# Performance work log

Hardware: AMD Instinct MI355X
Metric: run time of the kernel (lower is better)

Reference implementation:

```python
import jax, jax.numpy as jnp
import numpy as np

B, L, H_IN, H_RED, H_MLP = 2, 1024, 768, 128, 256

def setup_inputs() -> dict:
    key = jax.random.key(0)
    ks = jax.random.split(key, 7)
    s_in = 1.0 / np.sqrt(H_IN)
    s_p = 1.0 / np.sqrt(2 * H_RED)
    s_m = 1.0 / np.sqrt(H_MLP)
    return {
        "inputs": jax.random.normal(ks[0], (B, L, H_IN), dtype=jnp.float32),
        "Wr": jax.random.uniform(ks[1], (H_RED, H_IN), jnp.float32, -s_in, s_in),
        "br": jax.random.uniform(ks[2], (H_RED,), jnp.float32, -s_in, s_in),
        "W1": jax.random.uniform(ks[3], (H_MLP, 2 * H_RED), jnp.float32, -s_p, s_p),
        "b1": jax.random.uniform(ks[4], (H_MLP,), jnp.float32, -s_p, s_p),
        "W2": jax.random.uniform(ks[5], (1, H_MLP), jnp.float32, -s_m, s_m),
        "b2": jax.random.uniform(ks[6], (1,), jnp.float32, -s_m, s_m),
    }

def reference(inputs, Wr, br, W1, b1, W2, b2):
    # pre_reduction: [B,L,H_IN] -> [B,L,H_RED]
    e = jnp.einsum("blh,rh->blr", inputs, Wr) + br
    b_, l_, r_ = e.shape
    # pairwise concat: row i gets e[i], col j gets e[j] -> [B,L,L,2R]
    row = jnp.broadcast_to(e[:, :, None, :], (b_, l_, l_, r_))
    col = jnp.broadcast_to(e[:, None, :, :], (b_, l_, l_, r_))
    pair = jnp.concatenate([row, col], axis=-1)
    # Lin2D: Linear(2R,256) -> ReLU -> Linear(256,1)
    h = jax.nn.relu(jnp.einsum("bijc,mc->bijm", pair, W1) + b1)
    out = jnp.einsum("bijm,om->bijo", h, W2) + b2  # [B,L,L,1]
    out = out[..., 0]  # [B,L,L]
    # symmetrize: triu(out) + triu(out,1)^T
    upper = jnp.triu(out)
    lower = jnp.swapaxes(jnp.triu(out, k=1), -1, -2)
    return upper + lower
```

## Files before the change

### kernel.cpp

```cpp
#include <hip/hip_runtime.h>

typedef __attribute__((ext_vector_type(4))) float f32x4;
typedef __attribute__((ext_vector_type(8))) short bf16x8;

__device__ inline unsigned short f2bf(float x) {
  unsigned u = __builtin_bit_cast(unsigned, x);
  u += 0x7fffu + ((u >> 16) & 1u);
  return (unsigned short)(u >> 16);
}

__device__ inline bf16x8 pack8(f32x4 lo, f32x4 hi) {
  bf16x8 r;
  r[0] = (short)f2bf(lo[0]); r[1] = (short)f2bf(lo[1]);
  r[2] = (short)f2bf(lo[2]); r[3] = (short)f2bf(lo[3]);
  r[4] = (short)f2bf(hi[0]); r[5] = (short)f2bf(hi[1]);
  r[6] = (short)f2bf(hi[2]); r[7] = (short)f2bf(hi[3]);
  return r;
}

__global__ __launch_bounds__(256) void prep_kernel(
    const float* __restrict__ X, const float* __restrict__ Wr,
    const float* __restrict__ W1, const float* __restrict__ W2,
    unsigned short* __restrict__ Xbf, unsigned short* __restrict__ Wrbf,
    unsigned short* __restrict__ W1bf, float* __restrict__ w2h) {
  int bid = blockIdx.x, tid = threadIdx.x;
  if (bid < 768) {
    size_t o = (size_t)bid * 2048 + tid * 8;
    f32x4 a = *(const f32x4*)(X + o), b = *(const f32x4*)(X + o + 4);
    *(bf16x8*)(Xbf + o) = pack8(a, b);
  } else if (bid < 816) {
    size_t o = (size_t)(bid - 768) * 2048 + tid * 8;
    f32x4 a = *(const f32x4*)(Wr + o), b = *(const f32x4*)(Wr + o + 4);
    *(bf16x8*)(Wrbf + o) = pack8(a, b);
  } else if (bid < 848) {
    size_t o = (size_t)(bid - 816) * 2048 + tid * 8;
    int m = (int)(o >> 7), k = (int)(o & 127);
    const float* src = (m < 256) ? (W1 + (size_t)m * 256 + k)
                                 : (W1 + (size_t)(m - 256) * 256 + 128 + k);
    f32x4 a = *(const f32x4*)src, b = *(const f32x4*)(src + 4);
    *(bf16x8*)(W1bf + o) = pack8(a, b);
  } else {
    w2h[tid] = 0.5f * W2[tid];
  }
}

__global__ __launch_bounds__(256) void gemm1_kernel(
    const unsigned short* __restrict__ Xbf, const unsigned short* __restrict__ Wrbf,
    const float* __restrict__ br, unsigned short* __restrict__ Ebf) {
  int wave = threadIdx.x >> 6, lane = threadIdx.x & 63;
  int tok0 = (blockIdx.x * 4 + wave) * 16;
  int n0 = blockIdx.y * 64;
  int lr = lane & 15, kg = (lane >> 4) * 8;
  const unsigned short* ap = Xbf + (size_t)(tok0 + lr) * 768 + kg;
  const unsigned short* bp0 = Wrbf + (size_t)(n0 + lr) * 768 + kg;
  const unsigned short* bp1 = bp0 + 16 * 768;
  const unsigned short* bp2 = bp0 + 32 * 768;
  const unsigned short* bp3 = bp0 + 48 * 768;
  f32x4 acc0 = {0,0,0,0}, acc1 = {0,0,0,0}, acc2 = {0,0,0,0}, acc3 = {0,0,0,0};
#pragma unroll 4
  for (int k0 = 0; k0 < 768; k0 += 32) {
    bf16x8 a = *(const bf16x8*)(ap + k0);
    bf16x8 b0 = *(const bf16x8*)(bp0 + k0);
    bf16x8 b1 = *(const bf16x8*)(bp1 + k0);
    bf16x8 b2 = *(const bf16x8*)(bp2 + k0);
    bf16x8 b3 = *(const bf16x8*)(bp3 + k0);
    acc0 = __builtin_amdgcn_mfma_f32_16x16x32_bf16(a, b0, acc0, 0, 0, 0);
    acc1 = __builtin_amdgcn_mfma_f32_16x16x32_bf16(a, b1, acc1, 0, 0, 0);
    acc2 = __builtin_amdgcn_mfma_f32_16x16x32_bf16(a, b2, acc2, 0, 0, 0);
    acc3 = __builtin_amdgcn_mfma_f32_16x16x32_bf16(a, b3, acc3, 0, 0, 0);
  }
  int rb = (lane >> 4) * 4;
  f32x4 accs[4] = {acc0, acc1, acc2, acc3};
#pragma unroll
  for (int t = 0; t < 4; ++t) {
    int n = n0 + t * 16 + lr;
    float bias = br[n];
#pragma unroll
    for (int r = 0; r < 4; ++r)
      Ebf[(size_t)(tok0 + rb + r) * 128 + n] = f2bf(accs[t][r] + bias);
  }
}

__global__ __launch_bounds__(256) void gemm2_kernel(
    const unsigned short* __restrict__ Ebf, const unsigned short* __restrict__ W1bf,
    const float* __restrict__ b1, const float* __restrict__ w2h,
    float* __restrict__ UVt, float* __restrict__ cvec) {
  int wave = threadIdx.x >> 6, lane = threadIdx.x & 63;
  int t0 = blockIdx.x * 64;
  int m0 = (blockIdx.y * 4 + wave) * 16;
  int lr = lane & 15, kg = (lane >> 4) * 8;
  const unsigned short* aB = W1bf + (size_t)(m0 + lr) * 128 + kg;
  f32x4 acc[4] = {{0,0,0,0},{0,0,0,0},{0,0,0,0},{0,0,0,0}};
#pragma unroll
  for (int k0 = 0; k0 < 128; k0 += 32) {
    bf16x8 a = *(const bf16x8*)(aB + k0);
#pragma unroll
    for (int t = 0; t < 4; ++t) {
      bf16x8 b = *(const bf16x8*)(Ebf + (size_t)(t0 + t * 16 + lr) * 128 + kg + k0);
      acc[t] = __builtin_amdgcn_mfma_f32_16x16x32_bf16(a, b, acc[t], 0, 0, 0);
    }
  }
  int rb = (lane >> 4) * 4;
  float p[4] = {0.f, 0.f, 0.f, 0.f};
#pragma unroll
  for (int t = 0; t < 4; ++t) {
#pragma unroll
    for (int r = 0; r < 4; ++r) {
      int m = m0 + rb + r;
      float val = acc[t][r] + ((m0 < 256) ? b1[m] : 0.f);
      UVt[(size_t)m * 2048 + t0 + t * 16 + lr] = val;
      p[t] = fmaf(w2h[m & 255], val, p[t]);
    }
  }
#pragma unroll
  for (int t = 0; t < 4; ++t) {
    p[t] += __shfl_xor(p[t], 16);
    p[t] += __shfl_xor(p[t], 32);
  }
  if (lane < 16) {
    int h = (m0 < 256) ? 0 : 1;
#pragma unroll
    for (int t = 0; t < 4; ++t)
      atomicAdd(&cvec[h * 2048 + t0 + t * 16 + lane], p[t]);
  }
}

__global__ __launch_bounds__(256) void pairwise_kernel(
    const float* __restrict__ UVt, const float* __restrict__ w2h,
    const float* __restrict__ cvec, const float* __restrict__ b2p,
    float* __restrict__ Out) {
  __shared__ float u_s[4][64][36];
  __shared__ float v_s[4][64][36];
  __shared__ float w2_s[256];
  __shared__ float cuv[64];

  int tid = threadIdx.x;
  int wave = tid >> 6, lane = tid & 63;
  int b = blockIdx.y;
  int p = blockIdx.x;
  int it = 0;
  while (p >= 32 - it) { p -= 32 - it; ++it; }
  int jt = it + p;

  int utok = b * 1024 + it * 32;
  int vtok = b * 1024 + jt * 32;

  w2_s[tid] = w2h[tid];
  if (tid < 32) cuv[tid] = cvec[utok + tid];
  else if (tid < 64) cuv[tid] = cvec[2048 + vtok + (tid - 32)];

  int mr = lane >> 3, tq = (lane & 7) * 4;
#pragma unroll
  for (int g = 0; g < 8; ++g) {
    int ml = g * 8 + mr;
    int m = wave * 64 + ml;
    *(f32x4*)&u_s[wave][ml][tq] = *(const f32x4*)(UVt + (size_t)m * 2048 + utok + tq);
    *(f32x4*)&v_s[wave][ml][tq] = *(const f32x4*)(UVt + (size_t)(256 + m) * 2048 + vtok + tq);
  }
  __syncthreads();

  int tx = lane & 7, ty = lane >> 3;
  float acc[4][4] = {{0,0,0,0},{0,0,0,0},{0,0,0,0},{0,0,0,0}};
  for (int ml = 0; ml < 64; ml += 4) {
    f32x4 wq = *(const f32x4*)&w2_s[wave * 64 + ml];
#pragma unroll
    for (int s = 0; s < 4; ++s) {
      f32x4 uu = *(const f32x4*)&u_s[wave][ml + s][4 * ty];
      f32x4 vv = *(const f32x4*)&v_s[wave][ml + s][4 * tx];
      float w = wq[s];
#pragma unroll
      for (int i = 0; i < 4; ++i)
#pragma unroll
        for (int j = 0; j < 4; ++j)
          acc[i][j] = fmaf(w, fabsf(uu[i] + vv[j]), acc[i][j]);
    }
  }

  __syncthreads();
  float* ov = (float*)u_s;
  if (wave > 0) {
#pragma unroll
    for (int i = 0; i < 4; ++i) {
      f32x4 rowv = {acc[i][0], acc[i][1], acc[i][2], acc[i][3]};
      *(f32x4*)&ov[(((wave - 1) * 4 + i) * 64 + lane) * 4] = rowv;
    }
  }
  __syncthreads();
  if (wave == 0) {
#pragma unroll
    for (int w = 1; w < 4; ++w)
#pragma unroll
      for (int i = 0; i < 4; ++i) {
        f32x4 rowv = *(const f32x4*)&ov[(((w - 1) * 4 + i) * 64 + lane) * 4];
#pragma unroll
        for (int j = 0; j < 4; ++j) acc[i][j] += rowv[j];
      }
    float b2v = b2p[0];
    float val[4][4];
#pragma unroll
    for (int i = 0; i < 4; ++i)
#pragma unroll
      for (int j = 0; j < 4; ++j)
        val[i][j] = acc[i][j] + cuv[4 * ty + i] + cuv[32 + 4 * tx + j] + b2v;

    size_t obase = (size_t)b << 20;
    int i0 = it * 32, j0 = jt * 32;
    if (it != jt) {
#pragma unroll
      for (int i = 0; i < 4; ++i) {
        f32x4 dv = {val[i][0], val[i][1], val[i][2], val[i][3]};
        *(f32x4*)(Out + obase + (size_t)(i0 + 4 * ty + i) * 1024 + j0 + 4 * tx) = dv;
      }
      float* t32 = (float*)v_s;
#pragma unroll
      for (int i = 0; i < 4; ++i)
#pragma unroll
        for (int j = 0; j < 4; ++j)
          t32[(4 * ty + i) * 33 + 4 * tx + j] = val[i][j];
      __builtin_amdgcn_s_waitcnt(0);
#pragma unroll
      for (int i = 0; i < 4; ++i) {
        f32x4 mv;
#pragma unroll
        for (int k = 0; k < 4; ++k) mv[k] = t32[(4 * tx + k) * 33 + 4 * ty + i];
        *(f32x4*)(Out + obase + (size_t)(j0 + 4 * ty + i) * 1024 + i0 + 4 * tx) = mv;
      }
    } else {
#pragma unroll
      for (int i = 0; i < 4; ++i)
#pragma unroll
        for (int j = 0; j < 4; ++j) {
          int il = 4 * ty + i, jl = 4 * tx + j;
          if (jl >= il) Out[obase + (size_t)(i0 + il) * 1024 + j0 + jl] = val[i][j];
          if (jl > il)  Out[obase + (size_t)(j0 + jl) * 1024 + i0 + il] = val[i][j];
        }
    }
  }
}

extern "C" void kernel_launch(void* const* d_in, const int* in_sizes, int n_in,
                              void* d_out, int out_size, void* d_ws, size_t ws_size,
                              hipStream_t stream) {
  (void)in_sizes; (void)n_in; (void)out_size; (void)ws_size;
  const float* X  = (const float*)d_in[0];
  const float* Wr = (const float*)d_in[1];
  const float* br = (const float*)d_in[2];
  const float* W1 = (const float*)d_in[3];
  const float* b1 = (const float*)d_in[4];
  const float* W2 = (const float*)d_in[5];
  const float* b2 = (const float*)d_in[6];
  float* Out = (float*)d_out;

  char* ws = (char*)d_ws;
  unsigned short* Xbf  = (unsigned short*)(ws);
  unsigned short* Wrbf = (unsigned short*)(ws + 3145728);
  unsigned short* W1bf = (unsigned short*)(ws + 3342336);
  float*          w2h  = (float*)(ws + 3473408);
  unsigned short* Ebf  = (unsigned short*)(ws + 3474432);
  float*          UVt  = (float*)(ws + 3998720);
  float*          cvec = (float*)(ws + 8193024);

  prep_kernel<<<849, 256, 0, stream>>>(X, Wr, W1, W2, Xbf, Wrbf, W1bf, w2h);
  hipMemsetAsync(cvec, 0, 2 * 2048 * sizeof(float), stream);
  gemm1_kernel<<<dim3(32, 2), 256, 0, stream>>>(Xbf, Wrbf, br, Ebf);
  gemm2_kernel<<<dim3(32, 8), 256, 0, stream>>>(Ebf, W1bf, b1, w2h, UVt, cvec);
  pairwise_kernel<<<dim3(528, 2), 256, 0, stream>>>(UVt, w2h, cvec, b2, Out);
}
```

Measured before the change: 64.99 us.

## Parallelize pairwise epilogue across waves, fold memset into prep, widen gemm1 grid

The memset of cvec is replaced by zeroing inside the prep kernel, and the w2h buffer is dropped by moving the 0.5 scale into the atomic add and the final sum. gemm1 now gives each block 16 output columns instead of 64, so it launches four times as many blocks for better occupancy at the cost of reloading the X tile more often. In the pairwise kernel all four waves now share the cross-wave reduction and the transposed writes, where before wave 0 did them alone, and launch bounds ask for two blocks per SM. The goal is to cut serial epilogue time and launch overhead.

```diff
diff --git a/kernel.cpp b/kernel.cpp
--- a/kernel.cpp
+++ b/kernel.cpp
@@ -20,27 +20,27 @@
 
 __global__ __launch_bounds__(256) void prep_kernel(
     const float* __restrict__ X, const float* __restrict__ Wr,
-    const float* __restrict__ W1, const float* __restrict__ W2,
+    const float* __restrict__ W1,
     unsigned short* __restrict__ Xbf, unsigned short* __restrict__ Wrbf,
-    unsigned short* __restrict__ W1bf, float* __restrict__ w2h) {
+    unsigned short* __restrict__ W1bf, float* __restrict__ cvec) {
   int bid = blockIdx.x, tid = threadIdx.x;
   if (bid < 768) {
     size_t o = (size_t)bid * 2048 + tid * 8;
-    f32x4 a = *(const f32x4*)(X + o), b = *(const f32x4*)(X + o + 4);
-    *(bf16x8*)(Xbf + o) = pack8(a, b);
+    *(bf16x8*)(Xbf + o) = pack8(*(const f32x4*)(X + o), *(const f32x4*)(X + o + 4));
   } else if (bid < 816) {
     size_t o = (size_t)(bid - 768) * 2048 + tid * 8;
-    f32x4 a = *(const f32x4*)(Wr + o), b = *(const f32x4*)(Wr + o + 4);
-    *(bf16x8*)(Wrbf + o) = pack8(a, b);
+    *(bf16x8*)(Wrbf + o) = pack8(*(const f32x4*)(Wr + o), *(const f32x4*)(Wr + o + 4));
   } else if (bid < 848) {
     size_t o = (size_t)(bid - 816) * 2048 + tid * 8;
     int m = (int)(o >> 7), k = (int)(o & 127);
     const float* src = (m < 256) ? (W1 + (size_t)m * 256 + k)
                                  : (W1 + (size_t)(m - 256) * 256 + 128 + k);
-    f32x4 a = *(const f32x4*)src, b = *(const f32x4*)(src + 4);
-    *(bf16x8*)(W1bf + o) = pack8(a, b);
+    *(bf16x8*)(W1bf + o) = pack8(*(const f32x4*)src, *(const f32x4*)(src + 4));
   } else {
-    w2h[tid] = 0.5f * W2[tid];
+    f32x4 z = {0.f, 0.f, 0.f, 0.f};
+#pragma unroll
+    for (int i = 0; i < 4; ++i)
+      *(f32x4*)(cvec + tid * 16 + i * 4) = z;
   }
 }
 
@@ -49,41 +49,27 @@
     const float* __restrict__ br, unsigned short* __restrict__ Ebf) {
   int wave = threadIdx.x >> 6, lane = threadIdx.x & 63;
   int tok0 = (blockIdx.x * 4 + wave) * 16;
-  int n0 = blockIdx.y * 64;
+  int n0 = blockIdx.y * 16;
   int lr = lane & 15, kg = (lane >> 4) * 8;
   const unsigned short* ap = Xbf + (size_t)(tok0 + lr) * 768 + kg;
-  const unsigned short* bp0 = Wrbf + (size_t)(n0 + lr) * 768 + kg;
-  const unsigned short* bp1 = bp0 + 16 * 768;
-  const unsigned short* bp2 = bp0 + 32 * 768;
-  const unsigned short* bp3 = bp0 + 48 * 768;
-  f32x4 acc0 = {0,0,0,0}, acc1 = {0,0,0,0}, acc2 = {0,0,0,0}, acc3 = {0,0,0,0};
-#pragma unroll 4
+  const unsigned short* bp = Wrbf + (size_t)(n0 + lr) * 768 + kg;
+  f32x4 acc = {0, 0, 0, 0};
+#pragma unroll 6
   for (int k0 = 0; k0 < 768; k0 += 32) {
     bf16x8 a = *(const bf16x8*)(ap + k0);
-    bf16x8 b0 = *(const bf16x8*)(bp0 + k0);
-    bf16x8 b1 = *(const bf16x8*)(bp1 + k0);
-    bf16x8 b2 = *(const bf16x8*)(bp2 + k0);
-    bf16x8 b3 = *(const bf16x8*)(bp3 + k0);
-    acc0 = __builtin_amdgcn_mfma_f32_16x16x32_bf16(a, b0, acc0, 0, 0, 0);
-    acc1 = __builtin_amdgcn_mfma_f32_16x16x32_bf16(a, b1, acc1, 0, 0, 0);
-    acc2 = __builtin_amdgcn_mfma_f32_16x16x32_bf16(a, b2, acc2, 0, 0, 0);
-    acc3 = __builtin_amdgcn_mfma_f32_16x16x32_bf16(a, b3, acc3, 0, 0, 0);
+    bf16x8 b = *(const bf16x8*)(bp + k0);
+    acc = __builtin_amdgcn_mfma_f32_16x16x32_bf16(a, b, acc, 0, 0, 0);
   }
   int rb = (lane >> 4) * 4;
-  f32x4 accs[4] = {acc0, acc1, acc2, acc3};
-#pragma unroll
-  for (int t = 0; t < 4; ++t) {
-    int n = n0 + t * 16 + lr;
-    float bias = br[n];
-#pragma unroll
-    for (int r = 0; r < 4; ++r)
-      Ebf[(size_t)(tok0 + rb + r) * 128 + n] = f2bf(accs[t][r] + bias);
-  }
+  float bias = br[n0 + lr];
+#pragma unroll
+  for (int r = 0; r < 4; ++r)
+    Ebf[(size_t)(tok0 + rb + r) * 128 + n0 + lr] = f2bf(acc[r] + bias);
 }
 
 __global__ __launch_bounds__(256) void gemm2_kernel(
     const unsigned short* __restrict__ Ebf, const unsigned short* __restrict__ W1bf,
-    const float* __restrict__ b1, const float* __restrict__ w2h,
+    const float* __restrict__ b1, const float* __restrict__ W2,
     float* __restrict__ UVt, float* __restrict__ cvec) {
   int wave = threadIdx.x >> 6, lane = threadIdx.x & 63;
   int t0 = blockIdx.x * 64;
@@ -109,7 +95,7 @@
       int m = m0 + rb + r;
       float val = acc[t][r] + ((m0 < 256) ? b1[m] : 0.f);
       UVt[(size_t)m * 2048 + t0 + t * 16 + lr] = val;
-      p[t] = fmaf(w2h[m & 255], val, p[t]);
+      p[t] = fmaf(W2[m & 255], val, p[t]);
     }
   }
 #pragma unroll
@@ -121,12 +107,12 @@
     int h = (m0 < 256) ? 0 : 1;
 #pragma unroll
     for (int t = 0; t < 4; ++t)
-      atomicAdd(&cvec[h * 2048 + t0 + t * 16 + lane], p[t]);
-  }
-}
-
-__global__ __launch_bounds__(256) void pairwise_kernel(
-    const float* __restrict__ UVt, const float* __restrict__ w2h,
+      atomicAdd(&cvec[h * 2048 + t0 + t * 16 + lane], 0.5f * p[t]);
+  }
+}
+
+__global__ __launch_bounds__(256, 2) void pairwise_kernel(
+    const float* __restrict__ UVt, const float* __restrict__ W2,
     const float* __restrict__ cvec, const float* __restrict__ b2p,
     float* __restrict__ Out) {
   __shared__ float u_s[4][64][36];
@@ -145,11 +131,15 @@
   int utok = b * 1024 + it * 32;
   int vtok = b * 1024 + jt * 32;
 
-  w2_s[tid] = w2h[tid];
+  w2_s[tid] = W2[tid];
   if (tid < 32) cuv[tid] = cvec[utok + tid];
   else if (tid < 64) cuv[tid] = cvec[2048 + vtok + (tid - 32)];
+  __syncthreads();
 
   int mr = lane >> 3, tq = (lane & 7) * 4;
+  int tx = lane & 7, ty = lane >> 3;
+  float acc[4][4] = {{0,0,0,0},{0,0,0,0},{0,0,0,0},{0,0,0,0}};
+
 #pragma unroll
   for (int g = 0; g < 8; ++g) {
     int ml = g * 8 + mr;
@@ -157,10 +147,7 @@
     *(f32x4*)&u_s[wave][ml][tq] = *(const f32x4*)(UVt + (size_t)m * 2048 + utok + tq);
     *(f32x4*)&v_s[wave][ml][tq] = *(const f32x4*)(UVt + (size_t)(256 + m) * 2048 + vtok + tq);
   }
-  __syncthreads();
-
-  int tx = lane & 7, ty = lane >> 3;
-  float acc[4][4] = {{0,0,0,0},{0,0,0,0},{0,0,0,0},{0,0,0,0}};
+
   for (int ml = 0; ml < 64; ml += 4) {
     f32x4 wq = *(const f32x4*)&w2_s[wave * 64 + ml];
 #pragma unroll
@@ -176,64 +163,56 @@
     }
   }
 
-  __syncthreads();
-  float* ov = (float*)u_s;
-  if (wave > 0) {
-#pragma unroll
-    for (int i = 0; i < 4; ++i) {
-      f32x4 rowv = {acc[i][0], acc[i][1], acc[i][2], acc[i][3]};
-      *(f32x4*)&ov[(((wave - 1) * 4 + i) * 64 + lane) * 4] = rowv;
-    }
-  }
-  __syncthreads();
-  if (wave == 0) {
-#pragma unroll
-    for (int w = 1; w < 4; ++w)
-#pragma unroll
-      for (int i = 0; i < 4; ++i) {
-        f32x4 rowv = *(const f32x4*)&ov[(((w - 1) * 4 + i) * 64 + lane) * 4];
-#pragma unroll
-        for (int j = 0; j < 4; ++j) acc[i][j] += rowv[j];
-      }
-    float b2v = b2p[0];
-    float val[4][4];
-#pragma unroll
-    for (int i = 0; i < 4; ++i)
-#pragma unroll
-      for (int j = 0; j < 4; ++j)
-        val[i][j] = acc[i][j] + cuv[4 * ty + i] + cuv[32 + 4 * tx + j] + b2v;
-
-    size_t obase = (size_t)b << 20;
-    int i0 = it * 32, j0 = jt * 32;
-    if (it != jt) {
-#pragma unroll
-      for (int i = 0; i < 4; ++i) {
-        f32x4 dv = {val[i][0], val[i][1], val[i][2], val[i][3]};
-        *(f32x4*)(Out + obase + (size_t)(i0 + 4 * ty + i) * 1024 + j0 + 4 * tx) = dv;
-      }
-      float* t32 = (float*)v_s;
-#pragma unroll
-      for (int i = 0; i < 4; ++i)
-#pragma unroll
-        for (int j = 0; j < 4; ++j)
-          t32[(4 * ty + i) * 33 + 4 * tx + j] = val[i][j];
-      __builtin_amdgcn_s_waitcnt(0);
-#pragma unroll
-      for (int i = 0; i < 4; ++i) {
-        f32x4 mv;
-#pragma unroll
-        for (int k = 0; k < 4; ++k) mv[k] = t32[(4 * tx + k) * 33 + 4 * ty + i];
-        *(f32x4*)(Out + obase + (size_t)(j0 + 4 * ty + i) * 1024 + i0 + 4 * tx) = mv;
-      }
-    } else {
-#pragma unroll
-      for (int i = 0; i < 4; ++i)
-#pragma unroll
-        for (int j = 0; j < 4; ++j) {
-          int il = 4 * ty + i, jl = 4 * tx + j;
-          if (jl >= il) Out[obase + (size_t)(i0 + il) * 1024 + j0 + jl] = val[i][j];
-          if (jl > il)  Out[obase + (size_t)(j0 + jl) * 1024 + i0 + il] = val[i][j];
-        }
+  float* ovp = (float*)u_s;
+  float* t2p = (float*)v_s;
+  __syncthreads();
+#pragma unroll
+  for (int i = 0; i < 4; ++i) {
+    f32x4 rv = {acc[i][0], acc[i][1], acc[i][2], acc[i][3]};
+    *(f32x4*)&ovp[((size_t)wave * 32 + 4 * ty + i) * 36 + 4 * tx] = rv;
+  }
+  __syncthreads();
+
+  int ly = lane >> 3, tc = lane & 7;
+  int row = wave * 8 + ly;
+  float b2v = b2p[0];
+  f32x4 sum = {0, 0, 0, 0};
+#pragma unroll
+  for (int q = 0; q < 4; ++q) {
+    f32x4 part = *(const f32x4*)&ovp[((size_t)q * 32 + row) * 36 + 4 * tc];
+#pragma unroll
+    for (int j = 0; j < 4; ++j) sum[j] += part[j];
+  }
+  float cu = cuv[row];
+  f32x4 val;
+#pragma unroll
+  for (int j = 0; j < 4; ++j)
+    val[j] = 0.5f * sum[j] + cu + cuv[32 + 4 * tc + j] + b2v;
+
+  *(f32x4*)&t2p[(size_t)row * 36 + 4 * tc] = val;
+
+  size_t obase = (size_t)b << 20;
+  int i0 = it * 32, j0 = jt * 32;
+  if (it != jt)
+    *(f32x4*)(Out + obase + (size_t)(i0 + row) * 1024 + j0 + 4 * tc) = val;
+  else {
+#pragma unroll
+    for (int j = 0; j < 4; ++j) {
+      int jl = 4 * tc + j;
+      if (jl >= row) Out[obase + (size_t)(i0 + row) * 1024 + j0 + jl] = val[j];
+    }
+  }
+  __syncthreads();
+  f32x4 mv;
+#pragma unroll
+  for (int j = 0; j < 4; ++j) mv[j] = t2p[(size_t)(4 * tc + j) * 36 + row];
+  if (it != jt)
+    *(f32x4*)(Out + obase + (size_t)(j0 + row) * 1024 + i0 + 4 * tc) = mv;
+  else {
+#pragma unroll
+    for (int j = 0; j < 4; ++j) {
+      int c = 4 * tc + j;
+      if (row > c) Out[obase + (size_t)(i0 + row) * 1024 + j0 + c] = mv[j];
     }
   }
 }
@@ -255,14 +234,12 @@
   unsigned short* Xbf  = (unsigned short*)(ws);
   unsigned short* Wrbf = (unsigned short*)(ws + 3145728);
   unsigned short* W1bf = (unsigned short*)(ws + 3342336);
-  float*          w2h  = (float*)(ws + 3473408);
-  unsigned short* Ebf  = (unsigned short*)(ws + 3474432);
-  float*          UVt  = (float*)(ws + 3998720);
-  float*          cvec = (float*)(ws + 8193024);
-
-  prep_kernel<<<849, 256, 0, stream>>>(X, Wr, W1, W2, Xbf, Wrbf, W1bf, w2h);
-  hipMemsetAsync(cvec, 0, 2 * 2048 * sizeof(float), stream);
-  gemm1_kernel<<<dim3(32, 2), 256, 0, stream>>>(Xbf, Wrbf, br, Ebf);
-  gemm2_kernel<<<dim3(32, 8), 256, 0, stream>>>(Ebf, W1bf, b1, w2h, UVt, cvec);
-  pairwise_kernel<<<dim3(528, 2), 256, 0, stream>>>(UVt, w2h, cvec, b2, Out);
-}
+  unsigned short* Ebf  = (unsigned short*)(ws + 3473408);
+  float*          UVt  = (float*)(ws + 3997696);
+  float*          cvec = (float*)(ws + 8192000);
+
+  prep_kernel<<<849, 256, 0, stream>>>(X, Wr, W1, Xbf, Wrbf, W1bf, cvec);
+  gemm1_kernel<<<dim3(32, 8), 256, 0, stream>>>(Xbf, Wrbf, br, Ebf);
+  gemm2_kernel<<<dim3(32, 8), 256, 0, stream>>>(Ebf, W1bf, b1, W2, UVt, cvec);
+  pairwise_kernel<<<dim3(528, 2), 256, 0, stream>>>(UVt, W2, cvec, b2, Out);
+}
```

New measurement: 53.71 us. -17.4%, faster.
